# Kernel optimization log

Hardware: AMD Instinct MI355X
Metric: run time of the kernel (lower is better)

Reference implementation:

```python
import jax, jax.numpy as jnp
import numpy as np

N_NODES = 50000
N_EDGES = 1600000
IN_FEATS = 256
OUT_FEATS = 128
NEG_SLOPE = 0.2


def setup_inputs() -> dict:
    key = jax.random.key(0)
    k1, k2, k3, k4, k5, k6 = jax.random.split(key, 6)
    gain = np.sqrt(2.0)  # calculate_gain('relu')
    w_std = gain * np.sqrt(2.0 / (IN_FEATS + OUT_FEATS))  # xavier normal
    a_std = gain * np.sqrt(2.0 / (1 + OUT_FEATS))
    return {
        "feat": jax.random.normal(k1, (N_NODES, IN_FEATS), dtype=jnp.float32),
        "W": jax.random.normal(k2, (OUT_FEATS, IN_FEATS), dtype=jnp.float32) * w_std,
        "attn_l": jax.random.normal(k3, (1, OUT_FEATS), dtype=jnp.float32) * a_std,
        "attn_r": jax.random.normal(k4, (1, OUT_FEATS), dtype=jnp.float32) * a_std,
        "src": jax.random.randint(k5, (N_EDGES,), 0, N_NODES, dtype=jnp.int32),
        "dst": jax.random.randint(k6, (N_EDGES,), 0, N_NODES, dtype=jnp.int32),
    }


def reference(feat, W, attn_l, attn_r, src, dst):
    # h = fc(feat): [N, D]
    h = jnp.einsum("ni,di->nd", feat, W)
    # per-node attention logits
    el = jnp.sum(h * attn_l, axis=-1)  # [N]
    er = jnp.sum(h * attn_r, axis=-1)  # [N]
    # apply_edge: e_uv = el[u] + er[v], then leaky relu
    e = jax.nn.leaky_relu(el[src] + er[dst], NEG_SLOPE)  # [E]
    # edge softmax over incoming edges of each destination node
    m = jax.ops.segment_max(e, dst, num_segments=N_NODES)  # [N]
    m = jnp.where(jnp.isneginf(m), 0.0, m)  # nodes with no in-edges
    ex = jnp.exp(e - m[dst])  # [E]
    denom = jax.ops.segment_sum(ex, dst, num_segments=N_NODES)  # [N]
    alpha = ex / jnp.maximum(denom[dst], 1e-9)  # [E]
    # gspmv: rst[v] = sum_{(u->v)} alpha_uv * h[u]
    rst = jax.ops.segment_sum(h[src] * alpha[:, None], dst, num_segments=N_NODES)
    return rst
```

## Files before the change

kernel.cpp:

```cpp
#include <hip/hip_runtime.h>
#include <hip/hip_bf16.h>


#define IN_FEATS 256
#define OUT_FEATS 128
#define NBINS 256
#define CAPB_LOG 14
#define CAPB (1 << CAPB_LOG)
#define SCAT_BLOCKS 512

typedef __bf16 bf16x8 __attribute__((ext_vector_type(8)));
typedef float f32x4 __attribute__((ext_vector_type(4)));

__global__ void prep(const float* __restrict__ W, __bf16* __restrict__ Wb, int nw,
                     int* __restrict__ cur) {
    int i = blockIdx.x * 256 + threadIdx.x;
    if (i < nw) Wb[i] = (__bf16)W[i];
    if (i < NBINS) cur[i] = i << CAPB_LOG;
}

__global__ __launch_bounds__(256) void gemm_scatter(
    const float* __restrict__ feat, const __bf16* __restrict__ Wb,
    const float* __restrict__ attn_l, const float* __restrict__ attn_r,
    __bf16* __restrict__ hb, float* __restrict__ el, float* __restrict__ er,
    const int* __restrict__ src, const int* __restrict__ dst,
    int* __restrict__ bin_cur, unsigned* __restrict__ arena,
    int n, int E, int G) {
    __shared__ int h[NBINS];
    __shared__ int base[NBINS];

    if (blockIdx.x >= G) {
        const int blk = blockIdx.x - G;
        const int t = threadIdx.x;
        h[t] = 0;
        __syncthreads();
        const int chunk = (E + SCAT_BLOCKS - 1) / SCAT_BLOCKS;
        const int beg = blk * chunk;
        const int end = min(beg + chunk, E);
        for (int i = beg + t; i < end; i += 256)
            atomicAdd(&h[dst[i] >> 8], 1);
        __syncthreads();
        if (h[t] > 0)
            base[t] = atomicAdd(&bin_cur[t], h[t]);
        h[t] = 0;
        __syncthreads();
        for (int i = beg + t; i < end; i += 256) {
            int d = dst[i];
            int bin = d >> 8;
            int pos = base[bin] + atomicAdd(&h[bin], 1);
            pos = min(pos, ((bin + 1) << CAPB_LOG) - 1);
            arena[pos] = ((unsigned)d << 16) | (unsigned)src[i];
        }
        return;
    }

    const int wid = threadIdx.x >> 6;
    const int lane = threadIdx.x & 63;
    const int s = lane & 15;
    const int q = lane >> 4;
    const int m0 = blockIdx.x * 64 + wid * 16;
    if (m0 >= n) return;

    const int mrow = min(m0 + s, n - 1);
    const float* arow = feat + (size_t)mrow * IN_FEATS + q * 8;

    f32x4 acc[8];
#pragma unroll
    for (int nt = 0; nt < 8; nt++) acc[nt] = (f32x4){0.f, 0.f, 0.f, 0.f};

#pragma unroll
    for (int ks = 0; ks < 8; ks++) {
        const int k0 = ks * 32;
        float4 f0 = *(const float4*)(arow + k0);
        float4 f1 = *(const float4*)(arow + k0 + 4);
        bf16x8 a;
        a[0] = (__bf16)f0.x; a[1] = (__bf16)f0.y; a[2] = (__bf16)f0.z; a[3] = (__bf16)f0.w;
        a[4] = (__bf16)f1.x; a[5] = (__bf16)f1.y; a[6] = (__bf16)f1.z; a[7] = (__bf16)f1.w;
#pragma unroll
        for (int nt = 0; nt < 8; nt++) {
            bf16x8 b = *(const bf16x8*)(Wb + (size_t)(nt * 16 + s) * IN_FEATS + k0 + q * 8);
            acc[nt] = __builtin_amdgcn_mfma_f32_16x16x32_bf16(a, b, acc[nt], 0, 0, 0);
        }
    }

    float al[8], ar[8];
#pragma unroll
    for (int nt = 0; nt < 8; nt++) {
        al[nt] = attn_l[nt * 16 + s];
        ar[nt] = attn_r[nt * 16 + s];
    }

#pragma unroll
    for (int r = 0; r < 4; r++) {
        const int row = m0 + q * 4 + r;
        const bool ok = row < n;
        float pl = 0.f, pr = 0.f;
#pragma unroll
        for (int nt = 0; nt < 8; nt++) {
            float v = acc[nt][r];
            if (ok) hb[(size_t)row * OUT_FEATS + nt * 16 + s] = (__bf16)v;
            pl += v * al[nt];
            pr += v * ar[nt];
        }
#pragma unroll
        for (int m = 1; m < 16; m <<= 1) {
            pl += __shfl_xor(pl, m);
            pr += __shfl_xor(pr, m);
        }
        if (ok && s == 0) {
            el[row] = pl;
            er[row] = pr;
        }
    }
}

__global__ __launch_bounds__(512) void build_csr(const unsigned* __restrict__ arena,
                                                 const int* __restrict__ bin_cur,
                                                 const float* __restrict__ el,
                                                 const float* __restrict__ er,
                                                 unsigned* __restrict__ edges,
                                                 int* __restrict__ row_beg,
                                                 int* __restrict__ row_end,
                                                 int N, int edges_cap) {
    __shared__ unsigned lds[CAPB];
    __shared__ int cnt[256];
    __shared__ int off[256];
    const int b = blockIdx.x;
    const int t = threadIdx.x;
    const int abeg = b << CAPB_LOG;
    const int cnt_in = min(bin_cur[b] - abeg, CAPB);

    for (int i = t; i < cnt_in; i += 512) lds[i] = arena[abeg + i];
    if (t < 256) cnt[t] = 0;
    __syncthreads();

    for (int i = t; i < cnt_in; i += 512)
        atomicAdd(&cnt[(lds[i] >> 16) & 255], 1);
    __syncthreads();
    if (t < 256) off[t] = cnt[t];
    __syncthreads();
    for (int o = 1; o < 256; o <<= 1) {
        int v = (t < 256 && t >= o) ? off[t - o] : 0;
        __syncthreads();
        if (t < 256) off[t] += v;
        __syncthreads();
    }
    int mycnt = 0, excl = 0;
    if (t < 256) {
        mycnt = cnt[t];
        excl = off[t] - mycnt;
    }
    __syncthreads();
    if (t < 256) {
        off[t] = excl;
        int v = (b << 8) + t;
        if (v < N) {
            row_beg[v] = abeg + excl;
            row_end[v] = abeg + excl + mycnt;
        }
        cnt[t] = 0;
    }
    __syncthreads();

    for (int i = t; i < cnt_in; i += 512) {
        unsigned e = lds[i];
        int d8 = (e >> 16) & 255;
        int u = (int)(e & 0xFFFFu);
        float x = el[u] + er[(b << 8) + d8];
        x = (x > 0.f) ? x : 0.2f * x;
        float w = __expf(x);
        int r = atomicAdd(&cnt[d8], 1);
        int pos = abeg + off[d8] + r;
        pos = min(pos, edges_cap - 1);
        edges[pos] = (__float_as_uint(w) & 0xFFFF0000u) | (unsigned)u;
    }
}

__global__ __launch_bounds__(256) void gat_kernel(const __bf16* __restrict__ hb,
                                                  const unsigned* __restrict__ edges,
                                                  const int* __restrict__ row_beg,
                                                  const int* __restrict__ row_end,
                                                  float* __restrict__ out, int n) {
    const int v = blockIdx.x * 4 + (threadIdx.x >> 6);
    if (v >= n) return;
    const int lane = threadIdx.x & 63;
    const int beg = row_beg[v];
    const int end = row_end[v];
    const unsigned* hbu = (const unsigned*)hb;

    float acc0 = 0.f, acc1 = 0.f, wsum = 0.f;
    for (int c0 = beg; c0 < end; c0 += 64) {
        const int nn = min(64, end - c0);
        int my = (c0 + lane < end) ? (int)edges[c0 + lane] : 0;

        int k = 0;
        for (; k + 8 <= nn; k += 8) {
#pragma unroll
            for (int tt = 0; tt < 8; tt++) {
                unsigned e = (unsigned)__shfl(my, k + tt);
                int u = (int)(e & 0xFFFFu);
                float w = __uint_as_float(e & 0xFFFF0000u);
                wsum += w;
                unsigned pair = hbu[(size_t)u * (OUT_FEATS / 2) + lane];
                acc0 += w * __uint_as_float(pair << 16);
                acc1 += w * __uint_as_float(pair & 0xffff0000u);
            }
        }
        for (; k < nn; k++) {
            unsigned e = (unsigned)__shfl(my, k);
            int u = (int)(e & 0xFFFFu);
            float w = __uint_as_float(e & 0xFFFF0000u);
            wsum += w;
            unsigned pair = hbu[(size_t)u * (OUT_FEATS / 2) + lane];
            acc0 += w * __uint_as_float(pair << 16);
            acc1 += w * __uint_as_float(pair & 0xffff0000u);
        }
    }
    const float dnm = fmaxf(wsum, 1e-9f);
    float2 o = make_float2(acc0 / dnm, acc1 / dnm);
    *(float2*)(out + (size_t)v * OUT_FEATS + lane * 2) = o;
}

extern "C" void kernel_launch(void* const* d_in, const int* in_sizes, int n_in,
                              void* d_out, int out_size, void* d_ws, size_t ws_size,
                              hipStream_t stream) {
    const float* feat   = (const float*)d_in[0];
    const float* W      = (const float*)d_in[1];
    const float* attn_l = (const float*)d_in[2];
    const float* attn_r = (const float*)d_in[3];
    const int*   src    = (const int*)d_in[4];
    const int*   dst    = (const int*)d_in[5];
    const int N = in_sizes[0] / IN_FEATS;
    const int E = in_sizes[4];
    float* out = (float*)d_out;

    char* p = (char*)d_ws;
    auto alloc = [&](size_t bytes) -> char* {
        char* r = p;
        p += (bytes + 255) & ~(size_t)255;
        return r;
    };
    const int nbuckets = (N + 255) / 256;
    const int edges_cap = nbuckets * CAPB;

    __bf16* hb    = (__bf16*)alloc((size_t)N * OUT_FEATS * sizeof(__bf16));
    __bf16* Wb    = (__bf16*)alloc((size_t)OUT_FEATS * IN_FEATS * sizeof(__bf16));
    float* el     = (float*)alloc((size_t)N * sizeof(float));
    float* er     = (float*)alloc((size_t)N * sizeof(float));
    int*   bin_cur = (int*)alloc((size_t)NBINS * sizeof(int));
    int*   row_beg = (int*)alloc((size_t)N * sizeof(int));
    int*   row_end = (int*)alloc((size_t)N * sizeof(int));
    unsigned* arena = (unsigned*)alloc((size_t)NBINS * CAPB * sizeof(unsigned));
    unsigned* edges = (unsigned*)alloc((size_t)edges_cap * sizeof(unsigned));

    prep<<<dim3((OUT_FEATS * IN_FEATS + 255) / 256), dim3(256), 0, stream>>>(
        W, Wb, OUT_FEATS * IN_FEATS, bin_cur);

    const int G = (N + 63) / 64;
    gemm_scatter<<<dim3(G + SCAT_BLOCKS), dim3(256), 0, stream>>>(
        feat, Wb, attn_l, attn_r, hb, el, er, src, dst, bin_cur, arena, N, E, G);

    build_csr<<<dim3(nbuckets), dim3(512), 0, stream>>>(arena, bin_cur, el, er, edges,
                                                        row_beg, row_end, N, edges_cap);

    gat_kernel<<<dim3((N + 3) / 4), dim3(256), 0, stream>>>(hb, edges, row_beg,
                                                            row_end, out, N);
}
```

Measured before the change: 212.6 us.

## Replace two-level bucketed CSR build with global degree histogram, scan, and atomic placement

```diff
diff --git a/kernel.cpp b/kernel.cpp
--- a/kernel.cpp
+++ b/kernel.cpp
@@ -4,56 +4,64 @@
 
 #define IN_FEATS 256
 #define OUT_FEATS 128
-#define NBINS 256
-#define CAPB_LOG 14
-#define CAPB (1 << CAPB_LOG)
-#define SCAT_BLOCKS 512
 
 typedef __bf16 bf16x8 __attribute__((ext_vector_type(8)));
 typedef float f32x4 __attribute__((ext_vector_type(4)));
 
 __global__ void prep(const float* __restrict__ W, __bf16* __restrict__ Wb, int nw,
-                     int* __restrict__ cur) {
+                     int* __restrict__ deg, int* __restrict__ cur, int N) {
     int i = blockIdx.x * 256 + threadIdx.x;
     if (i < nw) Wb[i] = (__bf16)W[i];
-    if (i < NBINS) cur[i] = i << CAPB_LOG;
-}
-
-__global__ __launch_bounds__(256) void gemm_scatter(
+    if (i < N) { deg[i] = 0; cur[i] = 0; }
+}
+
+__global__ __launch_bounds__(256) void hist(const int* __restrict__ dst,
+                                            int* __restrict__ deg, int E) {
+    const int stride = gridDim.x * 256;
+    for (int i = blockIdx.x * 256 + threadIdx.x; i < E; i += stride)
+        atomicAdd(&deg[dst[i]], 1);
+}
+
+__global__ __launch_bounds__(256) void scanA(const int* __restrict__ deg,
+                                             int* __restrict__ row_loc,
+                                             int* __restrict__ bsum, int N) {
+    __shared__ int s[256];
+    const int t = threadIdx.x;
+    const int v = blockIdx.x * 256 + t;
+    const int d = (v < N) ? deg[v] : 0;
+    s[t] = d;
+    __syncthreads();
+    for (int o = 1; o < 256; o <<= 1) {
+        int x = (t >= o) ? s[t - o] : 0;
+        __syncthreads();
+        s[t] += x;
+        __syncthreads();
+    }
+    if (v < N) row_loc[v] = s[t] - d;
+    if (t == 255) bsum[blockIdx.x] = s[255];
+}
+
+__global__ __launch_bounds__(256) void scanB(const int* __restrict__ bsum,
+                                             int* __restrict__ bbase, int nb) {
+    __shared__ int s[256];
+    const int t = threadIdx.x;
+    const int d = (t < nb) ? bsum[t] : 0;
+    s[t] = d;
+    __syncthreads();
+    for (int o = 1; o < 256; o <<= 1) {
+        int x = (t >= o) ? s[t - o] : 0;
+        __syncthreads();
+        s[t] += x;
+        __syncthreads();
+    }
+    if (t < nb) bbase[t] = s[t] - d;
+}
+
+__global__ __launch_bounds__(256) void gemm(
     const float* __restrict__ feat, const __bf16* __restrict__ Wb,
     const float* __restrict__ attn_l, const float* __restrict__ attn_r,
     __bf16* __restrict__ hb, float* __restrict__ el, float* __restrict__ er,
-    const int* __restrict__ src, const int* __restrict__ dst,
-    int* __restrict__ bin_cur, unsigned* __restrict__ arena,
-    int n, int E, int G) {
-    __shared__ int h[NBINS];
-    __shared__ int base[NBINS];
-
-    if (blockIdx.x >= G) {
-        const int blk = blockIdx.x - G;
-        const int t = threadIdx.x;
-        h[t] = 0;
-        __syncthreads();
-        const int chunk = (E + SCAT_BLOCKS - 1) / SCAT_BLOCKS;
-        const int beg = blk * chunk;
-        const int end = min(beg + chunk, E);
-        for (int i = beg + t; i < end; i += 256)
-            atomicAdd(&h[dst[i] >> 8], 1);
-        __syncthreads();
-        if (h[t] > 0)
-            base[t] = atomicAdd(&bin_cur[t], h[t]);
-        h[t] = 0;
-        __syncthreads();
-        for (int i = beg + t; i < end; i += 256) {
-            int d = dst[i];
-            int bin = d >> 8;
-            int pos = base[bin] + atomicAdd(&h[bin], 1);
-            pos = min(pos, ((bin + 1) << CAPB_LOG) - 1);
-            arena[pos] = ((unsigned)d << 16) | (unsigned)src[i];
-        }
-        return;
-    }
-
+    int n) {
     const int wid = threadIdx.x >> 6;
     const int lane = threadIdx.x & 63;
     const int s = lane & 15;
@@ -114,104 +122,61 @@
     }
 }
 
-__global__ __launch_bounds__(512) void build_csr(const unsigned* __restrict__ arena,
-                                                 const int* __restrict__ bin_cur,
-                                                 const float* __restrict__ el,
-                                                 const float* __restrict__ er,
-                                                 unsigned* __restrict__ edges,
-                                                 int* __restrict__ row_beg,
-                                                 int* __restrict__ row_end,
-                                                 int N, int edges_cap) {
-    __shared__ unsigned lds[CAPB];
-    __shared__ int cnt[256];
-    __shared__ int off[256];
-    const int b = blockIdx.x;
-    const int t = threadIdx.x;
-    const int abeg = b << CAPB_LOG;
-    const int cnt_in = min(bin_cur[b] - abeg, CAPB);
-
-    for (int i = t; i < cnt_in; i += 512) lds[i] = arena[abeg + i];
-    if (t < 256) cnt[t] = 0;
-    __syncthreads();
-
-    for (int i = t; i < cnt_in; i += 512)
-        atomicAdd(&cnt[(lds[i] >> 16) & 255], 1);
-    __syncthreads();
-    if (t < 256) off[t] = cnt[t];
-    __syncthreads();
-    for (int o = 1; o < 256; o <<= 1) {
-        int v = (t < 256 && t >= o) ? off[t - o] : 0;
-        __syncthreads();
-        if (t < 256) off[t] += v;
-        __syncthreads();
-    }
-    int mycnt = 0, excl = 0;
-    if (t < 256) {
-        mycnt = cnt[t];
-        excl = off[t] - mycnt;
-    }
-    __syncthreads();
-    if (t < 256) {
-        off[t] = excl;
-        int v = (b << 8) + t;
-        if (v < N) {
-            row_beg[v] = abeg + excl;
-            row_end[v] = abeg + excl + mycnt;
-        }
-        cnt[t] = 0;
-    }
-    __syncthreads();
-
-    for (int i = t; i < cnt_in; i += 512) {
-        unsigned e = lds[i];
-        int d8 = (e >> 16) & 255;
-        int u = (int)(e & 0xFFFFu);
-        float x = el[u] + er[(b << 8) + d8];
+__global__ __launch_bounds__(256) void place(
+    const int* __restrict__ src, const int* __restrict__ dst,
+    const float* __restrict__ el, const float* __restrict__ er,
+    const int* __restrict__ row_loc, const int* __restrict__ bbase,
+    int* __restrict__ cur, unsigned* __restrict__ edges, int E) {
+    const int stride = gridDim.x * 256;
+    for (int i = blockIdx.x * 256 + threadIdx.x; i < E; i += stride) {
+        const int d = dst[i];
+        const int u = src[i];
+        float x = el[u] + er[d];
         x = (x > 0.f) ? x : 0.2f * x;
-        float w = __expf(x);
-        int r = atomicAdd(&cnt[d8], 1);
-        int pos = abeg + off[d8] + r;
-        pos = min(pos, edges_cap - 1);
+        const float w = __expf(x);
+        const int r = atomicAdd(&cur[d], 1);
+        const int pos = bbase[d >> 8] + row_loc[d] + r;
         edges[pos] = (__float_as_uint(w) & 0xFFFF0000u) | (unsigned)u;
     }
 }
 
 __global__ __launch_bounds__(256) void gat_kernel(const __bf16* __restrict__ hb,
                                                   const unsigned* __restrict__ edges,
-                                                  const int* __restrict__ row_beg,
-                                                  const int* __restrict__ row_end,
+                                                  const int* __restrict__ deg,
+                                                  const int* __restrict__ row_loc,
+                                                  const int* __restrict__ bbase,
                                                   float* __restrict__ out, int n) {
     const int v = blockIdx.x * 4 + (threadIdx.x >> 6);
     if (v >= n) return;
     const int lane = threadIdx.x & 63;
-    const int beg = row_beg[v];
-    const int end = row_end[v];
+    const int beg = __builtin_amdgcn_readfirstlane(bbase[v >> 8] + row_loc[v]);
+    const int end = __builtin_amdgcn_readfirstlane(beg + deg[v]);
     const unsigned* hbu = (const unsigned*)hb;
 
     float acc0 = 0.f, acc1 = 0.f, wsum = 0.f;
     for (int c0 = beg; c0 < end; c0 += 64) {
         const int nn = min(64, end - c0);
-        int my = (c0 + lane < end) ? (int)edges[c0 + lane] : 0;
+        unsigned my = (c0 + lane < end) ? edges[c0 + lane] : 0u;
 
         int k = 0;
         for (; k + 8 <= nn; k += 8) {
 #pragma unroll
             for (int tt = 0; tt < 8; tt++) {
-                unsigned e = (unsigned)__shfl(my, k + tt);
-                int u = (int)(e & 0xFFFFu);
+                unsigned e = (unsigned)__builtin_amdgcn_readlane((int)my, k + tt);
+                unsigned u = e & 0xFFFFu;
                 float w = __uint_as_float(e & 0xFFFF0000u);
+                unsigned pair = hbu[(size_t)u * (OUT_FEATS / 2) + lane];
                 wsum += w;
-                unsigned pair = hbu[(size_t)u * (OUT_FEATS / 2) + lane];
                 acc0 += w * __uint_as_float(pair << 16);
                 acc1 += w * __uint_as_float(pair & 0xffff0000u);
             }
         }
         for (; k < nn; k++) {
-            unsigned e = (unsigned)__shfl(my, k);
-            int u = (int)(e & 0xFFFFu);
+            unsigned e = (unsigned)__builtin_amdgcn_readlane((int)my, k);
+            unsigned u = e & 0xFFFFu;
             float w = __uint_as_float(e & 0xFFFF0000u);
+            unsigned pair = hbu[(size_t)u * (OUT_FEATS / 2) + lane];
             wsum += w;
-            unsigned pair = hbu[(size_t)u * (OUT_FEATS / 2) + lane];
             acc0 += w * __uint_as_float(pair << 16);
             acc1 += w * __uint_as_float(pair & 0xffff0000u);
         }
@@ -241,28 +206,33 @@
         return r;
     };
     const int nbuckets = (N + 255) / 256;
-    const int edges_cap = nbuckets * CAPB;
-
-    __bf16* hb    = (__bf16*)alloc((size_t)N * OUT_FEATS * sizeof(__bf16));
-    __bf16* Wb    = (__bf16*)alloc((size_t)OUT_FEATS * IN_FEATS * sizeof(__bf16));
-    float* el     = (float*)alloc((size_t)N * sizeof(float));
-    float* er     = (float*)alloc((size_t)N * sizeof(float));
-    int*   bin_cur = (int*)alloc((size_t)NBINS * sizeof(int));
-    int*   row_beg = (int*)alloc((size_t)N * sizeof(int));
-    int*   row_end = (int*)alloc((size_t)N * sizeof(int));
-    unsigned* arena = (unsigned*)alloc((size_t)NBINS * CAPB * sizeof(unsigned));
-    unsigned* edges = (unsigned*)alloc((size_t)edges_cap * sizeof(unsigned));
-
-    prep<<<dim3((OUT_FEATS * IN_FEATS + 255) / 256), dim3(256), 0, stream>>>(
-        W, Wb, OUT_FEATS * IN_FEATS, bin_cur);
+
+    __bf16* hb     = (__bf16*)alloc((size_t)N * OUT_FEATS * sizeof(__bf16));
+    __bf16* Wb     = (__bf16*)alloc((size_t)OUT_FEATS * IN_FEATS * sizeof(__bf16));
+    float*  el     = (float*)alloc((size_t)N * sizeof(float));
+    float*  er     = (float*)alloc((size_t)N * sizeof(float));
+    int*    deg    = (int*)alloc((size_t)N * sizeof(int));
+    int*    cur    = (int*)alloc((size_t)N * sizeof(int));
+    int*    row_loc = (int*)alloc((size_t)N * sizeof(int));
+    int*    bsum   = (int*)alloc(256 * sizeof(int));
+    int*    bbase  = (int*)alloc(256 * sizeof(int));
+    unsigned* edges = (unsigned*)alloc((size_t)E * sizeof(unsigned));
+
+    const int nw = OUT_FEATS * IN_FEATS;
+    const int pgrid = (max(nw, N) + 255) / 256;
+    prep<<<dim3(pgrid), dim3(256), 0, stream>>>(W, Wb, nw, deg, cur, N);
+
+    hist<<<dim3(1563), dim3(256), 0, stream>>>(dst, deg, E);
+
+    scanA<<<dim3(nbuckets), dim3(256), 0, stream>>>(deg, row_loc, bsum, N);
+    scanB<<<dim3(1), dim3(256), 0, stream>>>(bsum, bbase, nbuckets);
 
     const int G = (N + 63) / 64;
-    gemm_scatter<<<dim3(G + SCAT_BLOCKS), dim3(256), 0, stream>>>(
-        feat, Wb, attn_l, attn_r, hb, el, er, src, dst, bin_cur, arena, N, E, G);
-
-    build_csr<<<dim3(nbuckets), dim3(512), 0, stream>>>(arena, bin_cur, el, er, edges,
-                                                        row_beg, row_end, N, edges_cap);
-
-    gat_kernel<<<dim3((N + 3) / 4), dim3(256), 0, stream>>>(hb, edges, row_beg,
-                                                            row_end, out, N);
-}
+    gemm<<<dim3(G), dim3(256), 0, stream>>>(feat, Wb, attn_l, attn_r, hb, el, er, N);
+
+    place<<<dim3(1563), dim3(256), 0, stream>>>(src, dst, el, er, row_loc, bbase,
+                                                cur, edges, E);
+
+    gat_kernel<<<dim3((N + 3) / 4), dim3(256), 0, stream>>>(hb, edges, deg, row_loc,
+                                                            bbase, out, N);
+}
```

Result: slower. 339.0 us (+59.5%).
